# Optimization experiments

Hardware: AMD Instinct MI355X
Metric: run time of the kernel (lower is better)

The kernel has to match this reference:

```python
import jax, jax.numpy as jnp
import numpy as np
from jax import lax

D_MODEL = 1024
FFN = 4096
CHUNK = 256
TTT_LR = 0.01
KSIZE = 5


def setup_inputs() -> dict:
    key = jax.random.key(0)
    ks = jax.random.split(key, 7)
    B, T = 2, 4096
    x = jax.random.normal(ks[0], (B, T, D_MODEL), dtype=jnp.float32)
    ttt_target = jax.random.normal(ks[1], (B, T, D_MODEL), dtype=jnp.float32)
    w_gate_up = jax.random.normal(ks[2], (2 * FFN, D_MODEL), dtype=jnp.float32) * 0.02
    w_down = jax.random.normal(ks[3], (D_MODEL, FFN), dtype=jnp.float32) * 0.02
    ttt_proj = jax.random.normal(ks[4], (D_MODEL, D_MODEL), dtype=jnp.float32) * 0.02
    conv_w = jax.random.normal(ks[5], (D_MODEL, 1, KSIZE), dtype=jnp.float32) * 0.02
    conv_b = jax.random.normal(ks[6], (D_MODEL,), dtype=jnp.float32) * 0.02
    return {"x": x, "ttt_target": ttt_target, "w_gate_up": w_gate_up,
            "w_down": w_down, "ttt_proj": ttt_proj, "conv_w": conv_w, "conv_b": conv_b}


def _pad_and_chunk(a, chunk):
    B, T, D = a.shape
    pad = (-T) % chunk
    if pad:
        a = jnp.pad(a, ((0, 0), (0, pad), (0, 0)))
    return a.reshape(B, -1, chunk, D)


def reference(x, ttt_target, w_gate_up, w_down, ttt_proj, conv_w, conv_b):
    B, T, D = x.shape
    # SwiGLU up path
    gate_up = jnp.einsum('btd,fd->btf', x, w_gate_up)  # (B,T,2F)
    gate, up = jnp.split(gate_up, 2, axis=-1)
    h = jax.nn.silu(gate) * up  # (B,T,F)
    # causal depthwise conv on ttt_target (torch pads K-1 both sides then slices [:T])
    t_ncl = ttt_target.transpose(0, 2, 1)  # (B,D,T)
    t = lax.conv_general_dilated(
        t_ncl, conv_w, window_strides=(1,), padding=[(KSIZE - 1, 0)],
        dimension_numbers=('NCH', 'OIH', 'NCH'), feature_group_count=D)
    t = (t + conv_b[None, :, None]).transpose(0, 2, 1)  # (B,T,D)
    # chunk
    h_c = _pad_and_chunk(h, CHUNK)  # (B,nc,C,F)
    t_c = _pad_and_chunk(t, CHUNK)  # (B,nc,C,D)
    nc = h_c.shape[1]
    if nc > 1:
        t_proj = jnp.einsum('btcd,ed->btce', t_c[:, :-1], ttt_proj)  # (B,nc-1,C,D)
        d_down = jnp.einsum('btch,btcd->btdh', h_c[:, :-1], t_proj)  # (B,nc-1,D,F)
    else:
        d_down = jnp.zeros((B, 0, D, FFN), dtype=h.dtype)
    w_orig = jnp.broadcast_to(w_down[None, None], (B, 1, D, FFN))
    w_all = jnp.concatenate([w_orig, d_down * jnp.float32(TTT_LR)], axis=1)
    w_adapted = jnp.cumsum(w_all, axis=1)  # (B,nc,D,F)
    out = jnp.einsum('btdh,btch->btcd', w_adapted, h_c)  # (B,nc,C,D)
    return out.reshape(B, -1, D)[:, :T]
```

## Files before the change

kernel.cpp:

```cpp
#include <hip/hip_runtime.h>
#include <hip/hip_bf16.h>
#include <stdint.h>

typedef unsigned short ushort_t;
typedef __bf16 bf16x8 __attribute__((ext_vector_type(8)));
typedef float f32x16 __attribute__((ext_vector_type(16)));

#define BM 128
#define BN 128
#define BK 64

__device__ inline float b2f(ushort_t u) {
    unsigned int x = ((unsigned int)u) << 16;
    float f; __builtin_memcpy(&f, &x, 4); return f;
}
__device__ inline ushort_t f2b(float f) {
    unsigned int x; __builtin_memcpy(&x, &f, 4);
    unsigned int r = (x + 0x7FFFu + ((x >> 16) & 1u)) >> 16;
    return (ushort_t)r;
}
__device__ inline void stage16(const ushort_t* g, ushort_t* s) {
    __builtin_amdgcn_global_load_lds((const __attribute__((address_space(1))) void*)g,
                                     (__attribute__((address_space(3))) void*)s, 16, 0, 0);
}
__device__ inline int swz(int r) { return (r & 7) ^ ((r >> 3) & 3); }
__device__ inline void stage_tile(const ushort_t* G, int ld, int k0, ushort_t* S, int tid) {
#pragma unroll
    for (int t = 0; t < 4; ++t) {
        int e = tid + t * 256;
        int row = e >> 3;
        int sw = ((e & 7) ^ swz(row)) * 8;
        stage16(G + (long long)row * ld + k0 + sw, &S[e * 8]);
    }
}
__device__ inline bf16x8 ldfrag(const ushort_t* S, int r, int c) {
    return *(const bf16x8*)&S[r * BK + ((c ^ swz(r)) * 8)];
}
__device__ inline void tile_decode(int& m0, int& n0) {
    const int nx = gridDim.x;
    int lin = blockIdx.y * nx + blockIdx.x;
    if ((nx & 7) == 0) {
        int q = nx >> 3;
        int k = lin & 7, s = lin >> 3;
        n0 = (k * q + s % q) * BN;
        m0 = (s / q) * BM;
    } else {
        m0 = blockIdx.y * BM;
        n0 = blockIdx.x * BN;
    }
}


#define SBAR() __builtin_amdgcn_sched_barrier(0)
#define BARRIER() do { SBAR(); __builtin_amdgcn_s_barrier(); SBAR(); } while (0)
#define WAITV(N) asm volatile("s_waitcnt vmcnt(" #N ")" ::: "memory")

__device__ inline int sw2(int r) { return ((r) & 3) ^ ((r >> 3) & 3); }

__device__ inline void stage_half(const ushort_t* G, int ldg, int kElem,
                                  ushort_t* Sbuf, int h, int tid) {
#pragma unroll
    for (int i2 = 0; i2 < 2; ++i2) {
        int s = tid + i2 * 512;
        int r = s >> 2, q = s & 3;
        int c = 4 * h + (q ^ sw2(r));
        stage16(G + (long long)r * ldg + kElem + c * 8, Sbuf + h * 8192 + s * 8);
    }
}
__device__ inline bf16x8 ldfrag2(const ushort_t* Sbuf, int r, int c) {
    int h = c >> 2;
    int lp = (c ^ sw2(r)) & 3;
    return *(const bf16x8*)&Sbuf[h * 8192 + r * 32 + lp * 8];
}

template <int KS0, int MI0, bool LB>
__device__ __forceinline__ void phase_load(const ushort_t* cA, const ushort_t* cB,
                                           int wr, int wc, int l32, int hl,
                                           bf16x8 af_[2][2], bf16x8 bfr_[2][2]) {
#pragma unroll
    for (int k2 = 0; k2 < 2; ++k2) {
#pragma unroll
        for (int m2 = 0; m2 < 2; ++m2)
            af_[m2][k2] = ldfrag2(cA, wr * 128 + (MI0 + m2) * 32 + l32,
                                  (KS0 + k2) * 2 + hl);
        if (LB) {
#pragma unroll
            for (int n2 = 0; n2 < 2; ++n2)
                bfr_[n2][k2] = ldfrag2(cB, wc * 64 + n2 * 32 + l32,
                                       (KS0 + k2) * 2 + hl);
        }
    }
}
template <int KS0, int MI0>
__device__ __forceinline__ void phase_mfma(bf16x8 af_[2][2], bf16x8 bfr_[2][2],
                                           f32x16 (&acc)[4][2]) {
#pragma unroll
    for (int k2 = 0; k2 < 2; ++k2)
#pragma unroll
        for (int m2 = 0; m2 < 2; ++m2)
#pragma unroll
            for (int n2 = 0; n2 < 2; ++n2)
                acc[MI0 + m2][n2] = __builtin_amdgcn_mfma_f32_32x32x16_bf16(
                    af_[m2][k2], bfr_[n2][k2], acc[MI0 + m2][n2], 0, 0, 0);
}

__device__ __forceinline__ void gemm256_core(const ushort_t* __restrict__ Ag, int lda,
                                             const ushort_t* __restrict__ Bg, int ldb,
                                             int K, ushort_t* smem, int tid,
                                             int wr, int wc, int l32, int hl,
                                             f32x16 (&acc)[4][2]) {
    ushort_t* A0s = smem;
    ushort_t* A1s = smem + 16384;
    ushort_t* B0s = smem + 32768;
    ushort_t* B1s = smem + 49152;
    const int NT = K >> 6;

    stage_half(Ag, lda, 0, A0s, 0, tid);
    stage_half(Bg, ldb, 0, B0s, 0, tid);
    stage_half(Ag, lda, 0, A0s, 1, tid);
    stage_half(Bg, ldb, 0, B0s, 1, tid);
    stage_half(Ag, lda, 64, A1s, 0, tid);
    stage_half(Bg, ldb, 64, B1s, 0, tid);
    WAITV(8);
    BARRIER();

    for (int kt = 0; kt < NT; ++kt) {
        ushort_t* cA = (kt & 1) ? A1s : A0s;
        ushort_t* cB = (kt & 1) ? B1s : B0s;
        ushort_t* nA = (kt & 1) ? A0s : A1s;
        ushort_t* nB = (kt & 1) ? B0s : B1s;
        const bool h1 = (kt + 1 < NT), h2 = (kt + 2 < NT);
        const int kE1 = (kt + 1) << 6, kE2 = (kt + 2) << 6;
        bf16x8 af_[2][2], bfr_[2][2];
        if (h1) stage_half(Ag, lda, kE1, nA, 1, tid);
        phase_load<0, 0, true>(cA, cB, wr, wc, l32, hl, af_, bfr_);
        BARRIER();
        __builtin_amdgcn_s_setprio(1);
        phase_mfma<0, 0>(af_, bfr_, acc);
        __builtin_amdgcn_s_setprio(0);
        BARRIER();
        if (h1) stage_half(Bg, ldb, kE1, nB, 1, tid);
        phase_load<0, 2, false>(cA, cB, wr, wc, l32, hl, af_, bfr_);
        BARRIER();
        __builtin_amdgcn_s_setprio(1);
        phase_mfma<0, 2>(af_, bfr_, acc);
        __builtin_amdgcn_s_setprio(0);
        if (h1) { WAITV(8); } else { WAITV(0); }
        BARRIER();
        if (h2) stage_half(Ag, lda, kE2, cA, 0, tid);
        phase_load<2, 0, true>(cA, cB, wr, wc, l32, hl, af_, bfr_);
        BARRIER();
        __builtin_amdgcn_s_setprio(1);
        phase_mfma<2, 0>(af_, bfr_, acc);
        __builtin_amdgcn_s_setprio(0);
        BARRIER();
        if (h2) stage_half(Bg, ldb, kE2, cB, 0, tid);
        phase_load<2, 2, false>(cA, cB, wr, wc, l32, hl, af_, bfr_);
        BARRIER();
        __builtin_amdgcn_s_setprio(1);
        phase_mfma<2, 2>(af_, bfr_, acc);
        __builtin_amdgcn_s_setprio(0);
        if (h1) { if (h2) { WAITV(8); } else { WAITV(4); } }
        BARRIER();
    }
}

__global__ __launch_bounds__(512, 2)
void k_gemm256_silu(const ushort_t* __restrict__ A, const ushort_t* __restrict__ Bp,
                    ushort_t* __restrict__ H) {
    extern __shared__ __attribute__((aligned(16))) ushort_t smem2[];
    const int tid = threadIdx.x;
    const int lane = tid & 63, l32 = lane & 31, hl = lane >> 5;
    const int wv = tid >> 6, wr = wv >> 2, wc = wv & 3;
    int lin = blockIdx.y * 32 + blockIdx.x;
    int k8 = lin & 7, s = lin >> 3;
    int n0 = (k8 * 4 + (s & 3)) * 256;
    int m0 = (s >> 2) * 256;
    const ushort_t* Ag = A + (long long)m0 * 1024;
    const ushort_t* Bg = Bp + (long long)n0 * 1024;
    f32x16 acc[4][2];
#pragma unroll
    for (int i = 0; i < 4; ++i) { acc[i][0] = (f32x16)(0.f); acc[i][1] = (f32x16)(0.f); }
    gemm256_core(Ag, 1024, Bg, 1024, 1024, smem2, tid, wr, wc, l32, hl, acc);
    const int hc = (n0 >> 1) + wc * 32 + l32;
#pragma unroll
    for (int mi = 0; mi < 4; ++mi)
#pragma unroll
        for (int reg = 0; reg < 16; ++reg) {
            int row = m0 + wr * 128 + mi * 32 + (reg & 3) + 8 * (reg >> 2) + 4 * hl;
            float g = acc[mi][0][reg], u = acc[mi][1][reg];
            float sg = g / (1.f + __expf(-g));
            H[(long long)row * 4096 + hc] = f2b(sg * u);
        }
}

__global__ __launch_bounds__(512, 2)
void k_gemm256_tri(const ushort_t* __restrict__ Hh, ushort_t* __restrict__ P) {
    extern __shared__ __attribute__((aligned(16))) ushort_t smem2[];
    const int tid = threadIdx.x;
    const int lane = tid & 63, l32 = lane & 31, hl = lane >> 5;
    const int wv = tid >> 6, wr = wv >> 2, wc = wv & 3;
    int pairIdx = (blockIdx.x & 7) * 30 + (blockIdx.x >> 3);
    const int bb = pairIdx / 120;
    int p = pairIdx % 120;
    int i = 1, rem = p;
    while (rem >= i) { rem -= i; ++i; }
    const int j = rem;
    const ushort_t* Ag = Hh + (long long)bb * 4096 * 4096 + (long long)(i * 256) * 4096;
    const ushort_t* Bg = Hh + (long long)bb * 4096 * 4096 + (long long)(j * 256) * 4096;
    f32x16 acc[4][2];
#pragma unroll
    for (int a = 0; a < 4; ++a) { acc[a][0] = (f32x16)(0.f); acc[a][1] = (f32x16)(0.f); }
    gemm256_core(Ag, 4096, Bg, 4096, 4096, smem2, tid, wr, wc, l32, hl, acc);
    ushort_t* Pp = P + (long long)bb * 4096 * 4096;
#pragma unroll
    for (int mi = 0; mi < 4; ++mi)
#pragma unroll
        for (int nj = 0; nj < 2; ++nj) {
            int col = j * 256 + wc * 64 + nj * 32 + l32;
#pragma unroll
            for (int reg = 0; reg < 16; ++reg) {
                int row = i * 256 + wr * 128 + mi * 32 + (reg & 3) + 8 * (reg >> 2) + 4 * hl;
                Pp[(long long)row * 4096 + col] = f2b(acc[mi][nj][reg]);
            }
        }
}

__global__ void k_prep(const float* __restrict__ x, const float* __restrict__ wgu,
                       const float* __restrict__ proj, const float* __restrict__ wdown,
                       const float* __restrict__ tt, const float* __restrict__ cw,
                       const float* __restrict__ cb,
                       ushort_t* __restrict__ xb, ushort_t* __restrict__ gb,
                       ushort_t* __restrict__ pb, ushort_t* __restrict__ wb,
                       ushort_t* __restrict__ tb, int permW) {
    constexpr int T = 4096, D = 1024;
    int blk = blockIdx.x;
    if (blk < 21504) {
        int i = blk * 256 + threadIdx.x;
        const float* src; ushort_t* dst; int off; int dstoff;
        if (i < 2097152)      { src = x;     dst = xb; off = i; dstoff = off; }
        else if (i < 4194304) {
            src = wgu; dst = gb; off = i - 2097152;
            if (permW) {
                int r = off >> 8, cu = off & 255;
                int pr = (r < 4096) ? (((r >> 5) << 6) + (r & 31))
                                    : ((((r - 4096) >> 5) << 6) + 32 + ((r - 4096) & 31));
                dstoff = (pr << 8) + cu;
            } else dstoff = off;
        }
        else if (i < 4456448) { src = proj;  dst = pb; off = i - 4194304; dstoff = off; }
        else                  { src = wdown; dst = wb; off = i - 4456448; dstoff = off; }
        float4 v = ((const float4*)src)[off];
        ushort4 o; o.x = f2b(v.x); o.y = f2b(v.y); o.z = f2b(v.z); o.w = f2b(v.w);
        ((ushort4*)dst)[dstoff] = o;
    } else {
        int idx = (blk - 21504) * 256 + threadIdx.x;
        int d = idx % D;
        int t = (idx / D) % T;
        int b = idx / (D * T);
        float acc = cb[d];
#pragma unroll
        for (int k = 0; k < 5; ++k) {
            int ts = t - 4 + k;
            if (ts >= 0) acc += tt[(long long)b * T * D + (long long)ts * D + d] * cw[d * 5 + k];
        }
        tb[idx] = f2b(acc);
    }
}

__global__ __launch_bounds__(256, 4)
void k_gemm_nt(const ushort_t* __restrict__ A, const ushort_t* __restrict__ B,
               ushort_t* __restrict__ C, int K, int lda, int ldb, int ldc,
               long long sAb, long long sBb, long long sCb, float scale) {
    __shared__ __attribute__((aligned(16))) ushort_t sA[BM * BK];
    __shared__ __attribute__((aligned(16))) ushort_t sB[BN * BK];

    int m0, n0;
    tile_decode(m0, n0);
    const int bb = blockIdx.z;
    const ushort_t* Ab = A + bb * sAb + (long long)m0 * lda;
    const ushort_t* Bb = B + bb * sBb + (long long)n0 * ldb;

    const int tid = threadIdx.x;
    const int lane = tid & 63, l32 = lane & 31, half = lane >> 5;
    const int wave = tid >> 6;
    const int wm = (wave >> 1) * 64, wn = (wave & 1) * 64;

    f32x16 acc[2][2];
#pragma unroll
    for (int i = 0; i < 2; ++i)
#pragma unroll
        for (int j = 0; j < 2; ++j) acc[i][j] = (f32x16)(0.f);

    for (int k0 = 0; k0 < K; k0 += BK) {
        __syncthreads();
        stage_tile(Ab, lda, k0, sA, tid);
        stage_tile(Bb, ldb, k0, sB, tid);
        __syncthreads();
#pragma unroll
        for (int ks = 0; ks < 4; ++ks) {
            bf16x8 af[2], bfr[2];
#pragma unroll
            for (int mi = 0; mi < 2; ++mi)
                af[mi] = ldfrag(sA, wm + mi * 32 + l32, ks * 2 + half);
#pragma unroll
            for (int nj = 0; nj < 2; ++nj)
                bfr[nj] = ldfrag(sB, wn + nj * 32 + l32, ks * 2 + half);
#pragma unroll
            for (int mi = 0; mi < 2; ++mi)
#pragma unroll
                for (int nj = 0; nj < 2; ++nj)
                    acc[mi][nj] = __builtin_amdgcn_mfma_f32_32x32x16_bf16(af[mi], bfr[nj], acc[mi][nj], 0, 0, 0);
        }
    }

    ushort_t* Cp = C + bb * sCb;
#pragma unroll
    for (int mi = 0; mi < 2; ++mi)
#pragma unroll
        for (int nj = 0; nj < 2; ++nj) {
            int col = n0 + wn + nj * 32 + l32;
#pragma unroll
            for (int reg = 0; reg < 16; ++reg) {
                int row = m0 + wm + mi * 32 + (reg & 3) + 8 * (reg >> 2) + 4 * half;
                Cp[(long long)row * ldc + col] = f2b(acc[mi][nj][reg] * scale);
            }
        }
}

__global__ __launch_bounds__(256)
void k_gemm_silu(const ushort_t* __restrict__ A, const ushort_t* __restrict__ Bg,
                 const ushort_t* __restrict__ Bu, ushort_t* __restrict__ H,
                 int K, int lda, int ldb, int ldh) {
    __shared__ __attribute__((aligned(16))) ushort_t sA[BM * BK];
    __shared__ __attribute__((aligned(16))) ushort_t sBg[BN * BK];
    __shared__ __attribute__((aligned(16))) ushort_t sBu[BN * BK];

    int m0, n0;
    tile_decode(m0, n0);
    const ushort_t* Ab = A + (long long)m0 * lda;
    const ushort_t* Bgb = Bg + (long long)n0 * ldb;
    const ushort_t* Bub = Bu + (long long)n0 * ldb;

    const int tid = threadIdx.x;
    const int lane = tid & 63, l32 = lane & 31, half = lane >> 5;
    const int wave = tid >> 6;
    const int wm = (wave >> 1) * 64, wn = (wave & 1) * 64;

    f32x16 ag[2][2], au[2][2];
#pragma unroll
    for (int i = 0; i < 2; ++i)
#pragma unroll
        for (int j = 0; j < 2; ++j) { ag[i][j] = (f32x16)(0.f); au[i][j] = (f32x16)(0.f); }

    for (int k0 = 0; k0 < K; k0 += BK) {
        __syncthreads();
        stage_tile(Ab, lda, k0, sA, tid);
        stage_tile(Bgb, ldb, k0, sBg, tid);
        stage_tile(Bub, ldb, k0, sBu, tid);
        __syncthreads();
#pragma unroll
        for (int ks = 0; ks < 4; ++ks) {
            bf16x8 af[2], bg[2], bu[2];
#pragma unroll
            for (int mi = 0; mi < 2; ++mi)
                af[mi] = ldfrag(sA, wm + mi * 32 + l32, ks * 2 + half);
#pragma unroll
            for (int nj = 0; nj < 2; ++nj) {
                bg[nj] = ldfrag(sBg, wn + nj * 32 + l32, ks * 2 + half);
                bu[nj] = ldfrag(sBu, wn + nj * 32 + l32, ks * 2 + half);
            }
#pragma unroll
            for (int mi = 0; mi < 2; ++mi)
#pragma unroll
                for (int nj = 0; nj < 2; ++nj) {
                    ag[mi][nj] = __builtin_amdgcn_mfma_f32_32x32x16_bf16(af[mi], bg[nj], ag[mi][nj], 0, 0, 0);
                    au[mi][nj] = __builtin_amdgcn_mfma_f32_32x32x16_bf16(af[mi], bu[nj], au[mi][nj], 0, 0, 0);
                }
        }
    }

#pragma unroll
    for (int mi = 0; mi < 2; ++mi)
#pragma unroll
        for (int nj = 0; nj < 2; ++nj) {
            int col = n0 + wn + nj * 32 + l32;
#pragma unroll
            for (int reg = 0; reg < 16; ++reg) {
                int row = m0 + wm + mi * 32 + (reg & 3) + 8 * (reg >> 2) + 4 * half;
                float g = ag[mi][nj][reg], u = au[mi][nj][reg];
                float s = g / (1.f + __expf(-g));
                H[(long long)row * ldh + col] = f2b(s * u);
            }
        }
}

__global__ __launch_bounds__(256, 4)
void k_gemm_tri(const ushort_t* __restrict__ H, ushort_t* __restrict__ P,
                int K, int ldh, int ldp, long long sHb, long long sPb) {
    __shared__ __attribute__((aligned(16))) ushort_t sA[BM * BK];
    __shared__ __attribute__((aligned(16))) ushort_t sB[BN * BK];

    const int lin = blockIdx.x;
    const int g = lin >> 5, w = lin & 31;
    const int xk = w & 7, t = w >> 3;
    int pairIdx = g * 8 + xk;
    const int bb = pairIdx / 120;
    int p = pairIdx % 120;
    int i = 1, rem = p;
    while (rem >= i) { rem -= i; ++i; }
    const int j = rem;
    const int m0 = (t >> 1) * BM, n0 = (t & 1) * BN;

    const ushort_t* Ab = H + bb * sHb + (long long)(i * 256 + m0) * ldh;
    const ushort_t* Bb = H + bb * sHb + (long long)(j * 256 + n0) * ldh;

    const int tid = threadIdx.x;
    const int lane = tid & 63, l32 = lane & 31, half = lane >> 5;
    const int wave = tid >> 6;
    const int wm = (wave >> 1) * 64, wn = (wave & 1) * 64;

    f32x16 acc[2][2];
#pragma unroll
    for (int a = 0; a < 2; ++a)
#pragma unroll
        for (int c = 0; c < 2; ++c) acc[a][c] = (f32x16)(0.f);

    for (int k0 = 0; k0 < K; k0 += BK) {
        __syncthreads();
        stage_tile(Ab, ldh, k0, sA, tid);
        stage_tile(Bb, ldh, k0, sB, tid);
        __syncthreads();
#pragma unroll
        for (int ks = 0; ks < 4; ++ks) {
            bf16x8 af[2], bfr[2];
#pragma unroll
            for (int mi = 0; mi < 2; ++mi)
                af[mi] = ldfrag(sA, wm + mi * 32 + l32, ks * 2 + half);
#pragma unroll
            for (int nj = 0; nj < 2; ++nj)
                bfr[nj] = ldfrag(sB, wn + nj * 32 + l32, ks * 2 + half);
#pragma unroll
            for (int mi = 0; mi < 2; ++mi)
#pragma unroll
                for (int nj = 0; nj < 2; ++nj)
                    acc[mi][nj] = __builtin_amdgcn_mfma_f32_32x32x16_bf16(af[mi], bfr[nj], acc[mi][nj], 0, 0, 0);
        }
    }

    ushort_t* Pp = P + bb * sPb;
#pragma unroll
    for (int mi = 0; mi < 2; ++mi)
#pragma unroll
        for (int nj = 0; nj < 2; ++nj) {
            int col = j * 256 + n0 + wn + nj * 32 + l32;
#pragma unroll
            for (int reg = 0; reg < 16; ++reg) {
                int row = i * 256 + m0 + wm + mi * 32 + (reg & 3) + 8 * (reg >> 2) + 4 * half;
                Pp[(long long)row * ldp + col] = f2b(acc[mi][nj][reg]);
            }
        }
}

__global__ __launch_bounds__(256, 4)
void k_gemm_out(const ushort_t* __restrict__ h, const ushort_t* __restrict__ wdown,
                const ushort_t* __restrict__ P, const ushort_t* __restrict__ tpT,
                float* __restrict__ out) {
    constexpr int T = 4096, D = 1024, F = 4096, C = 256, K1 = 4096;
    __shared__ __attribute__((aligned(16))) ushort_t sA[BM * BK];
    __shared__ __attribute__((aligned(16))) ushort_t sB[BN * BK];

    const int z = blockIdx.z, bb = z >> 4, ii = z & 15;
    const int K2 = ii * C;
    int m0, n0;
    tile_decode(m0, n0);

    const ushort_t* A1 = h + (long long)bb * T * F + (long long)(ii * C + m0) * F;
    const ushort_t* B1 = wdown + (long long)n0 * F;
    const ushort_t* A2 = P + (long long)bb * T * T + (long long)(ii * C + m0) * T;
    const ushort_t* B2 = tpT + (long long)bb * D * T + (long long)n0 * T;

    const int tid = threadIdx.x;
    const int lane = tid & 63, l32 = lane & 31, half = lane >> 5;
    const int wave = tid >> 6;
    const int wm = (wave >> 1) * 64, wn = (wave & 1) * 64;

    f32x16 acc[2][2];
#pragma unroll
    for (int i = 0; i < 2; ++i)
#pragma unroll
        for (int j = 0; j < 2; ++j) acc[i][j] = (f32x16)(0.f);

    const int K = K1 + K2;
    for (int k0 = 0; k0 < K; k0 += BK) {
        const ushort_t* As = (k0 < K1) ? A1 + k0 : A2 + (k0 - K1);
        const ushort_t* Bs = (k0 < K1) ? B1 + k0 : B2 + (k0 - K1);
        __syncthreads();
        stage_tile(As, 4096, 0, sA, tid);
        stage_tile(Bs, 4096, 0, sB, tid);
        __syncthreads();
#pragma unroll
        for (int ks = 0; ks < 4; ++ks) {
            bf16x8 af[2], bfr[2];
#pragma unroll
            for (int mi = 0; mi < 2; ++mi)
                af[mi] = ldfrag(sA, wm + mi * 32 + l32, ks * 2 + half);
#pragma unroll
            for (int nj = 0; nj < 2; ++nj)
                bfr[nj] = ldfrag(sB, wn + nj * 32 + l32, ks * 2 + half);
#pragma unroll
            for (int mi = 0; mi < 2; ++mi)
#pragma unroll
                for (int nj = 0; nj < 2; ++nj)
                    acc[mi][nj] = __builtin_amdgcn_mfma_f32_32x32x16_bf16(af[mi], bfr[nj], acc[mi][nj], 0, 0, 0);
        }
    }

    float* Op = out + (long long)bb * T * D + (long long)ii * C * D;
#pragma unroll
    for (int mi = 0; mi < 2; ++mi)
#pragma unroll
        for (int nj = 0; nj < 2; ++nj) {
            int col = n0 + wn + nj * 32 + l32;
#pragma unroll
            for (int reg = 0; reg < 16; ++reg) {
                int row = m0 + wm + mi * 32 + (reg & 3) + 8 * (reg >> 2) + 4 * half;
                Op[(long long)row * D + col] = acc[mi][nj][reg];
            }
        }
}

static int g_big = -1;

extern "C" void kernel_launch(void* const* d_in, const int* in_sizes, int n_in,
                              void* d_out, int out_size, void* d_ws, size_t ws_size,
                              hipStream_t stream) {
    const float* x         = (const float*)d_in[0];
    const float* ttt_tgt   = (const float*)d_in[1];
    const float* w_gate_up = (const float*)d_in[2];
    const float* w_down    = (const float*)d_in[3];
    const float* ttt_proj  = (const float*)d_in[4];
    const float* conv_w    = (const float*)d_in[5];
    const float* conv_b    = (const float*)d_in[6];
    float* out = (float*)d_out;
    (void)in_sizes; (void)n_in; (void)out_size; (void)ws_size;

    constexpr int Bb = 2, T = 4096, D = 1024, F = 4096, C = 256;
    constexpr float LR = 0.01f;

    if (g_big < 0) {
        hipError_t e1 = hipFuncSetAttribute((const void*)k_gemm256_silu,
                                            hipFuncAttributeMaxDynamicSharedMemorySize, 131072);
        hipError_t e2 = hipFuncSetAttribute((const void*)k_gemm256_tri,
                                            hipFuncAttributeMaxDynamicSharedMemorySize, 131072);
        g_big = (e1 == hipSuccess && e2 == hipSuccess) ? 1 : 0;
    }

    char* ws = (char*)d_ws;
    ushort_t* x_bf     = (ushort_t*)(ws);
    ushort_t* wgu_bf   = (ushort_t*)(ws + 16777216LL);
    ushort_t* t_bf     = (ushort_t*)(ws + 2 * 16777216LL);
    ushort_t* P        = (ushort_t*)(ws);
    ushort_t* proj_bf  = (ushort_t*)(ws + 67108864LL);
    ushort_t* wdown_bf = (ushort_t*)(ws + 67108864LL + 2097152LL);
    ushort_t* tpT      = (ushort_t*)(ws + 67108864LL + 2097152LL + 8388608LL);
    ushort_t* h        = (ushort_t*)(ws + 67108864LL + 2097152LL + 8388608LL + 16777216LL);

    k_prep<<<21504 + 32768, 256, 0, stream>>>(x, w_gate_up, ttt_proj, w_down,
                                              ttt_tgt, conv_w, conv_b,
                                              x_bf, wgu_bf, proj_bf, wdown_bf, t_bf, g_big);

    k_gemm_nt<<<dim3(T / BN, D / BM, Bb), 256, 0, stream>>>(
        proj_bf, t_bf, tpT, D, D, D, T,
        0, (long long)T * D, (long long)D * T, LR);

    if (g_big) {
        k_gemm256_silu<<<dim3(32, 32, 1), 512, 131072, stream>>>(x_bf, wgu_bf, h);
    } else {
        k_gemm_silu<<<dim3(F / BN, (Bb * T) / BM, 1), 256, 0, stream>>>(
            x_bf, wgu_bf, wgu_bf + (long long)F * D, h, D, D, D, F);
    }

    if (g_big) {
        k_gemm256_tri<<<dim3(240, 1, 1), 512, 131072, stream>>>(h, P);
    } else {
        k_gemm_tri<<<dim3(960, 1, 1), 256, 0, stream>>>(
            h, P, F, F, T, (long long)T * F, (long long)T * T);
    }

    k_gemm_out<<<dim3(D / BN, C / BM, Bb * 16), 256, 0, stream>>>(
        h, wdown_bf, P, tpT, out);
}
```

Measured before the change: 626.3 us.

## Add 128x256-tile pipelined output GEMM with larger block and swizzled LDS

Replaces the final output GEMM (h·Wdown concatenated with P·tpT over a variable K) with a new 512-thread kernel using 128x256 tiles, double-buffered global_load_lds staging, MFMA 32x32x16 and setprio around the MFMA bursts. It launches 256 blocks remapped in groups of 8 so that blocks sharing an A panel run close together. The goal is more reuse per LDS load and compute overlapped with memory traffic, in place of the smaller 128x128 kernel. The trade-off is fewer blocks, a large 96KB LDS footprint, and imbalanced work because K grows with the chunk index.

```diff
diff --git a/kernel.cpp b/kernel.cpp
--- a/kernel.cpp
+++ b/kernel.cpp
@@ -67,10 +67,16 @@
         stage16(G + (long long)r * ldg + kElem + c * 8, Sbuf + h * 8192 + s * 8);
     }
 }
-__device__ inline bf16x8 ldfrag2(const ushort_t* Sbuf, int r, int c) {
+__device__ inline void stage_halfA(const ushort_t* G, int ldg,
+                                   ushort_t* Sbuf, int h, int tid) {
+    int r = tid >> 2, q = tid & 3;
+    int c = 4 * h + (q ^ sw2(r));
+    stage16(G + (long long)r * ldg + c * 8, Sbuf + h * 4096 + tid * 8);
+}
+__device__ inline bf16x8 ldfrag2(const ushort_t* Sbuf, int r, int c, int hs) {
     int h = c >> 2;
     int lp = (c ^ sw2(r)) & 3;
-    return *(const bf16x8*)&Sbuf[h * 8192 + r * 32 + lp * 8];
+    return *(const bf16x8*)&Sbuf[h * hs + r * 32 + lp * 8];
 }
 
 template <int KS0, int MI0, bool LB>
@@ -82,12 +88,12 @@
 #pragma unroll
         for (int m2 = 0; m2 < 2; ++m2)
             af_[m2][k2] = ldfrag2(cA, wr * 128 + (MI0 + m2) * 32 + l32,
-                                  (KS0 + k2) * 2 + hl);
+                                  (KS0 + k2) * 2 + hl, 8192);
         if (LB) {
 #pragma unroll
             for (int n2 = 0; n2 < 2; ++n2)
                 bfr_[n2][k2] = ldfrag2(cB, wc * 64 + n2 * 32 + l32,
-                                       (KS0 + k2) * 2 + hl);
+                                       (KS0 + k2) * 2 + hl, 8192);
         }
     }
 }
@@ -222,6 +228,125 @@
             for (int reg = 0; reg < 16; ++reg) {
                 int row = i * 256 + wr * 128 + mi * 32 + (reg & 3) + 8 * (reg >> 2) + 4 * hl;
                 Pp[(long long)row * 4096 + col] = f2b(acc[mi][nj][reg]);
+            }
+        }
+}
+
+__device__ __forceinline__ void oload_ks(const ushort_t* cA, const ushort_t* cB,
+                                         int ks0, int wr, int wc, int l32, int hl,
+                                         bf16x8 af_[2][2], bf16x8 bf_[2][2]) {
+#pragma unroll
+    for (int k2 = 0; k2 < 2; ++k2) {
+        int c = (ks0 + k2) * 2 + hl;
+#pragma unroll
+        for (int m2 = 0; m2 < 2; ++m2)
+            af_[m2][k2] = ldfrag2(cA, wr * 64 + m2 * 32 + l32, c, 4096);
+#pragma unroll
+        for (int n2 = 0; n2 < 2; ++n2)
+            bf_[n2][k2] = ldfrag2(cB, wc * 64 + n2 * 32 + l32, c, 8192);
+    }
+}
+__device__ __forceinline__ void omfma(bf16x8 af_[2][2], bf16x8 bf_[2][2],
+                                      f32x16 (&acc)[2][2]) {
+#pragma unroll
+    for (int k2 = 0; k2 < 2; ++k2)
+#pragma unroll
+        for (int m2 = 0; m2 < 2; ++m2)
+#pragma unroll
+            for (int n2 = 0; n2 < 2; ++n2)
+                acc[m2][n2] = __builtin_amdgcn_mfma_f32_32x32x16_bf16(
+                    af_[m2][k2], bf_[n2][k2], acc[m2][n2], 0, 0, 0);
+}
+
+__global__ __launch_bounds__(512, 2)
+void k_gemm256_out(const ushort_t* __restrict__ h, const ushort_t* __restrict__ wdown,
+                   const ushort_t* __restrict__ P, const ushort_t* __restrict__ tpT,
+                   float* __restrict__ out) {
+    constexpr int T = 4096, D = 1024, F = 4096, C = 256, K1 = 4096;
+    extern __shared__ __attribute__((aligned(16))) ushort_t smem2[];
+    const int tid = threadIdx.x;
+    const int lane = tid & 63, l32 = lane & 31, hl = lane >> 5;
+    const int wv = tid >> 6, wr = wv >> 2, wc = wv & 3;
+
+    const int bx = blockIdx.x;
+    const int logical = (bx & 7) * 32 + (bx >> 3);
+    const int z = logical >> 3, t = logical & 7;
+    const int bb = z >> 4, ii = z & 15;
+    const int m0 = (t >> 2) * 128, n0 = (t & 3) * 256;
+    const int K = K1 + ii * C;
+
+    const ushort_t* hA = h + (long long)bb * T * F + (long long)(ii * C + m0) * F;
+    const ushort_t* pA = P + (long long)bb * T * T + (long long)(ii * C + m0) * T;
+    const ushort_t* wB = wdown + (long long)n0 * F;
+    const ushort_t* tB = tpT + (long long)bb * D * T + (long long)n0 * T;
+
+    ushort_t* A0s = smem2;
+    ushort_t* A1s = smem2 + 8192;
+    ushort_t* B0s = smem2 + 16384;
+    ushort_t* B1s = smem2 + 32768;
+
+    f32x16 acc[2][2];
+#pragma unroll
+    for (int a = 0; a < 2; ++a)
+#pragma unroll
+        for (int c = 0; c < 2; ++c) acc[a][c] = (f32x16)(0.f);
+
+    auto srcA = [&](int kE) { return kE < K1 ? hA + kE : pA + (kE - K1); };
+    auto srcB = [&](int kE) { return kE < K1 ? wB + kE : tB + (kE - K1); };
+
+    const int NT = K >> 6;
+
+    stage_halfA(srcA(0), F, A0s, 0, tid);
+    stage_half (srcB(0), F, 0, B0s, 0, tid);
+    stage_halfA(srcA(0), F, A0s, 1, tid);
+    stage_half (srcB(0), F, 0, B0s, 1, tid);
+    stage_halfA(srcA(64), F, A1s, 0, tid);
+    stage_half (srcB(64), F, 0, B1s, 0, tid);
+    WAITV(6);
+    BARRIER();
+
+    for (int kt = 0; kt < NT; ++kt) {
+        ushort_t* cA = (kt & 1) ? A1s : A0s;
+        ushort_t* cB = (kt & 1) ? B1s : B0s;
+        ushort_t* nA = (kt & 1) ? A0s : A1s;
+        ushort_t* nB = (kt & 1) ? B0s : B1s;
+        const bool h1 = (kt + 1 < NT), h2 = (kt + 2 < NT);
+        const int kE1 = (kt + 1) << 6, kE2 = (kt + 2) << 6;
+        bf16x8 af_[2][2], bf_[2][2];
+        if (h1) {
+            stage_halfA(srcA(kE1), F, nA, 1, tid);
+            stage_half (srcB(kE1), F, 0, nB, 1, tid);
+        }
+        oload_ks(cA, cB, 0, wr, wc, l32, hl, af_, bf_);
+        BARRIER();
+        __builtin_amdgcn_s_setprio(1);
+        omfma(af_, bf_, acc);
+        __builtin_amdgcn_s_setprio(0);
+        if (h1) { WAITV(6); } else { WAITV(0); }
+        BARRIER();
+        if (h2) {
+            stage_halfA(srcA(kE2), F, cA, 0, tid);
+            stage_half (srcB(kE2), F, 0, cB, 0, tid);
+        }
+        oload_ks(cA, cB, 2, wr, wc, l32, hl, af_, bf_);
+        BARRIER();
+        __builtin_amdgcn_s_setprio(1);
+        omfma(af_, bf_, acc);
+        __builtin_amdgcn_s_setprio(0);
+        if (h2) { WAITV(6); } else { if (h1) { WAITV(3); } else { WAITV(0); } }
+        BARRIER();
+    }
+
+    float* Op = out + (long long)bb * T * D + (long long)(ii * C) * D;
+#pragma unroll
+    for (int mi = 0; mi < 2; ++mi)
+#pragma unroll
+        for (int nj = 0; nj < 2; ++nj) {
+            int col = n0 + wc * 64 + nj * 32 + l32;
+#pragma unroll
+            for (int reg = 0; reg < 16; ++reg) {
+                int row = m0 + wr * 64 + mi * 32 + (reg & 3) + 8 * (reg >> 2) + 4 * hl;
+                Op[(long long)row * D + col] = acc[mi][nj][reg];
             }
         }
 }
@@ -553,7 +678,9 @@
                                             hipFuncAttributeMaxDynamicSharedMemorySize, 131072);
         hipError_t e2 = hipFuncSetAttribute((const void*)k_gemm256_tri,
                                             hipFuncAttributeMaxDynamicSharedMemorySize, 131072);
-        g_big = (e1 == hipSuccess && e2 == hipSuccess) ? 1 : 0;
+        hipError_t e3 = hipFuncSetAttribute((const void*)k_gemm256_out,
+                                            hipFuncAttributeMaxDynamicSharedMemorySize, 98304);
+        g_big = (e1 == hipSuccess && e2 == hipSuccess && e3 == hipSuccess) ? 1 : 0;
     }
 
     char* ws = (char*)d_ws;
@@ -588,6 +715,10 @@
             h, P, F, F, T, (long long)T * F, (long long)T * T);
     }
 
-    k_gemm_out<<<dim3(D / BN, C / BM, Bb * 16), 256, 0, stream>>>(
-        h, wdown_bf, P, tpT, out);
-}
+    if (g_big) {
+        k_gemm256_out<<<dim3(256, 1, 1), 512, 98304, stream>>>(h, wdown_bf, P, tpT, out);
+    } else {
+        k_gemm_out<<<dim3(D / BN, C / BM, Bb * 16), 256, 0, stream>>>(
+            h, wdown_bf, P, tpT, out);
+    }
+}
```

After: 628.7 us. No clear change (+0.4%).
